# Kernel tuning notes

Hardware: AMD Instinct MI355X
Metric: run time of the kernel (lower is better)

## Reference

```python
import jax, jax.numpy as jnp
import numpy as np

NUM_HEADS = 8
MAX_POINTS = 8


def _sample_one(img, x, y):
    # img: [hd, Hs, Ws]; x, y: [N, P] pixel coords. Bilinear, zeros padding,
    # align_corners=True (caller already converted normalized coords to pixels).
    Hs, Ws = img.shape[-2], img.shape[-1]
    x0f = jnp.floor(x); y0f = jnp.floor(y)
    x0 = x0f.astype(jnp.int32); y0 = y0f.astype(jnp.int32)
    x1 = x0 + 1; y1 = y0 + 1
    wx1 = x - x0f; wx0 = 1.0 - wx1
    wy1 = y - y0f; wy0 = 1.0 - wy1

    def gather(yi, xi):
        valid = ((yi >= 0) & (yi < Hs) & (xi >= 0) & (xi < Ws)).astype(img.dtype)
        yc = jnp.clip(yi, 0, Hs - 1)
        xc = jnp.clip(xi, 0, Ws - 1)
        return img[:, yc, xc] * valid  # [hd, N, P]

    return (gather(y0, x0) * (wy0 * wx0) + gather(y0, x1) * (wy0 * wx1)
            + gather(y1, x0) * (wy1 * wx0) + gather(y1, x1) * (wy1 * wx1))


def _forward(query, ref, q_w, q_b, kv_w, kv_b, off_w, off_b, out_w, out_b, H, W, n_points):
    B, N, C = query.shape
    hd = C // NUM_HEADS
    scale = hd ** -0.5

    q = (query @ q_w + q_b).reshape(B, N, NUM_HEADS, hd)
    # kv_proj is dead code in the source forward (k, v are never used); params kept for parity.

    offsets = (query @ off_w + off_b).reshape(B, N, NUM_HEADS, MAX_POINTS, 2)
    offsets = offsets[:, :, :, :n_points]  # [B, N, nh, P, 2]

    ys = jnp.arange(H, dtype=query.dtype)
    xs = jnp.arange(W, dtype=query.dtype)
    coords = jnp.stack(jnp.meshgrid(ys, xs, indexing='ij'), -1).reshape(N, 2)  # (y, x)
    loc = coords[None, :, None, None, :] + offsets  # [B, N, nh, P, 2]
    g0 = loc[..., 0] / (H - 1) * 2.0 - 1.0
    g1 = loc[..., 1] / (W - 1) * 2.0 - 1.0
    # grid_sample reads grid[...,0] as x and grid[...,1] as y -> faithful to the
    # source's coordinate-channel ordering (channel 0 was normalized with H).
    x_pix = (g0 + 1.0) * 0.5 * (W - 1)
    y_pix = (g1 + 1.0) * 0.5 * (H - 1)

    ref_img = ref.reshape(B, C, H, W)  # faithful to source's .view (raw reinterpret, no permute)
    ref_heads = ref_img.reshape(B, NUM_HEADS, hd, H, W)  # per-head channel slice

    xb = x_pix.transpose(0, 2, 1, 3)  # [B, nh, N, P]
    yb = y_pix.transpose(0, 2, 1, 3)
    sampled = jax.vmap(jax.vmap(_sample_one))(ref_heads, xb, yb)  # [B, nh, hd, N, P]
    sampled = sampled.transpose(0, 3, 1, 4, 2)  # [B, N, nh, P, hd]

    attn = jax.nn.softmax(jnp.einsum('bnhd,bnhpd->bnhp', q, sampled) * scale, axis=-1)
    out = jnp.einsum('bnhp,bnhpd->bnhd', attn, sampled).reshape(B, N, C)
    return out @ out_w + out_b


def setup_inputs():
    key = jax.random.key(0)
    B, H, W, C = 4, 64, 64, 512
    N = H * W
    ks = jax.random.split(key, 8)
    w = lambda k, shp: jax.random.normal(k, shp, jnp.float32) * 0.02
    return {
        'query': jax.random.normal(ks[0], (B, N, C), jnp.float32),
        'ref': jax.random.normal(ks[1], (B, N, C), jnp.float32),
        'q_w': w(ks[2], (C, C)), 'q_b': jnp.zeros((C,), jnp.float32),
        'kv_w': w(ks[3], (C, 2 * C)), 'kv_b': jnp.zeros((2 * C,), jnp.float32),
        'off_w': w(ks[4], (C, NUM_HEADS * MAX_POINTS * 2)),
        'off_b': jnp.zeros((NUM_HEADS * MAX_POINTS * 2,), jnp.float32),
        'out_w': w(ks[5], (C, C)), 'out_b': jnp.zeros((C,), jnp.float32),
        'H': H, 'W': W, 'n_points': 8,
    }


def reference(query, ref, q_w, q_b, kv_w, kv_b, off_w, off_b, out_w, out_b, H, W, n_points):
    return _forward(query, ref, q_w, q_b, kv_w, kv_b, off_w, off_b, out_w, out_b, H, W, n_points)
```

## Files before the change

### kernel.cpp

```cpp
#include <hip/hip_runtime.h>
#include <cmath>

#define NUM_HEADS 8
#define MAX_POINTS 8
#define HD 64

typedef short bf16x8 __attribute__((ext_vector_type(8)));
typedef float f32x4 __attribute__((ext_vector_type(4)));
typedef float f32x2 __attribute__((ext_vector_type(2)));

typedef const __attribute__((address_space(1))) unsigned int gu32;
typedef __attribute__((address_space(3))) unsigned int lu32;

__device__ __forceinline__ unsigned short f2bf(float f) {
    unsigned u = __float_as_uint(f);
    unsigned r = (u + 0x7fff + ((u >> 16) & 1)) >> 16;
    return (unsigned short)r;
}
__device__ __forceinline__ unsigned packbf2(float a, float b) {
    return (unsigned)f2bf(a) | ((unsigned)f2bf(b) << 16);
}
__device__ __forceinline__ f32x2 bfpair(unsigned u) {
    f32x2 r;
    r.x = __uint_as_float(u << 16);
    r.y = __uint_as_float(u & 0xffff0000u);
    return r;
}
__device__ __forceinline__ f32x2 sp2(float v) { return (f32x2){v, v}; }
__device__ __forceinline__ f32x2 pkfma(f32x2 a, f32x2 b, f32x2 c) {
    f32x2 d;
    asm("v_pk_fma_f32 %0, %1, %2, %3" : "=v"(d) : "v"(a), "v"(b), "v"(c));
    return d;
}
__device__ __forceinline__ f32x2 pkmul(f32x2 a, f32x2 b) {
    f32x2 d;
    asm("v_pk_mul_f32 %0, %1, %2" : "=v"(d) : "v"(a), "v"(b));
    return d;
}

__global__ __launch_bounds__(256) void prep_k(
    const float* __restrict__ query, unsigned short* __restrict__ qin_bf,
    const float* __restrict__ ref, unsigned short* __restrict__ refT,
    const float* __restrict__ q_w, const float* __restrict__ off_w,
    const float* __restrict__ out_w, unsigned short* __restrict__ wcat,
    unsigned short* __restrict__ woutT)
{
    __shared__ float tile[32][33];
    int bid = blockIdx.x;
    int tid = threadIdx.x;

    if (bid < 8192) {
        int i = (bid * 256 + tid) * 4;
        float4 v = *(const float4*)&query[i];
        ushort4 o;
        o.x = f2bf(v.x); o.y = f2bf(v.y); o.z = f2bf(v.z); o.w = f2bf(v.w);
        *(ushort4*)&qin_bf[i] = o;
        return;
    }
    int tx = tid & 31, ty = tid >> 5;
    if (bid < 16384) {
        int b2 = bid - 8192;
        int z = b2 >> 11;
        int r = b2 & 2047;
        int k0 = (r & 15) * 32;
        int n0 = (r >> 4) * 32;
        size_t ib = (size_t)z * 512 * 4096;
#pragma unroll
        for (int i = 0; i < 32; i += 8)
            tile[ty + i][tx] = ref[ib + (size_t)(k0 + ty + i) * 4096 + n0 + tx];
        __syncthreads();
#pragma unroll
        for (int i = 0; i < 32; i += 8)
            refT[ib + (size_t)(n0 + ty + i) * 512 + k0 + tx] = f2bf(tile[tx][ty + i]);
        return;
    }
    int b3 = bid - 16384;
    int z = b3 >> 8;
    int r = b3 & 255;
    int k0 = (r & 15) * 32;
    int n0 = (r >> 4) * 32;
    const float* in; unsigned short* out; int N;
    if (z == 0)      { in = q_w;   out = wcat;             N = 512; }
    else if (z == 1) { in = off_w; out = wcat + 512 * 512; N = 128;
                       if (n0 >= 128) return; }
    else             { in = out_w; out = woutT;            N = 512; }
#pragma unroll
    for (int i = 0; i < 32; i += 8)
        tile[ty + i][tx] = in[(size_t)(k0 + ty + i) * N + n0 + tx];
    __syncthreads();
#pragma unroll
    for (int i = 0; i < 32; i += 8)
        out[(size_t)(n0 + ty + i) * 512 + k0 + tx] = f2bf(tile[tx][ty + i]);
}

__device__ __forceinline__ void gemm128_core(
    const unsigned short* A, const unsigned short* BT, int K,
    int bm, int bn, int tid, unsigned short* As, unsigned short* Bs,
    f32x4 (&acc)[4][4])
{
    int wave = tid >> 6, lane = tid & 63;
    int quad = lane >> 4, l16 = lane & 15;
    int wm = (wave >> 1) * 64, wn = (wave & 1) * 64;
    int srow = tid >> 2, sq = (tid & 3) * 8;
    const unsigned short* aP0 = &A[(size_t)(bm + srow) * K + sq];
    const unsigned short* aP1 = aP0 + (size_t)64 * K;
    const unsigned short* bP0 = &BT[(size_t)(bn + srow) * K + sq];
    const unsigned short* bP1 = bP0 + (size_t)64 * K;

#define STAGE(buf, k0)                                                         \
    do {                                                                       \
        lu32* aL0 = (lu32*)&As[(buf) * 4096 + wave * 512];                     \
        lu32* aL1 = (lu32*)&As[(buf) * 4096 + 2048 + wave * 512];              \
        lu32* bL0 = (lu32*)&Bs[(buf) * 4096 + wave * 512];                     \
        lu32* bL1 = (lu32*)&Bs[(buf) * 4096 + 2048 + wave * 512];              \
        __builtin_amdgcn_global_load_lds((gu32*)(aP0 + (k0)), aL0, 16, 0, 0);  \
        __builtin_amdgcn_global_load_lds((gu32*)(aP1 + (k0)), aL1, 16, 0, 0);  \
        __builtin_amdgcn_global_load_lds((gu32*)(bP0 + (k0)), bL0, 16, 0, 0);  \
        __builtin_amdgcn_global_load_lds((gu32*)(bP1 + (k0)), bL1, 16, 0, 0);  \
    } while (0)

    STAGE(0, 0);
    __syncthreads();
    int cur = 0;
    for (int k0 = 0; k0 < K; k0 += 32) {
        if (k0 + 32 < K) STAGE(cur ^ 1, k0 + 32);
        bf16x8 af[4], bfr[4];
#pragma unroll
        for (int t = 0; t < 4; ++t) {
            af[t]  = *(const bf16x8*)&As[cur * 4096 + (wm + t * 16 + l16) * 32 + quad * 8];
            bfr[t] = *(const bf16x8*)&Bs[cur * 4096 + (wn + t * 16 + l16) * 32 + quad * 8];
        }
#pragma unroll
        for (int mt = 0; mt < 4; ++mt)
#pragma unroll
            for (int nt = 0; nt < 4; ++nt)
                acc[mt][nt] = __builtin_amdgcn_mfma_f32_16x16x32_bf16(
                    af[mt], bfr[nt], acc[mt][nt], 0, 0, 0);
        __syncthreads();
        cur ^= 1;
    }
#undef STAGE
}

__global__ __launch_bounds__(256) void gemm_qoff_k(
    const unsigned short* __restrict__ A, const unsigned short* __restrict__ BT,
    const float* __restrict__ q_b, const float* __restrict__ off_b,
    unsigned short* __restrict__ qout, float* __restrict__ offout,
    int M, int K)
{
    __shared__ unsigned short As[2 * 128 * 32];
    __shared__ unsigned short Bs[2 * 128 * 32];
    int tid = threadIdx.x;
    int wave = tid >> 6, lane = tid & 63;
    int quad = lane >> 4, l16 = lane & 15;
    int bm = blockIdx.y * 128, bn = blockIdx.x * 128;
    int wm = (wave >> 1) * 64, wn = (wave & 1) * 64;

    f32x4 acc[4][4];
#pragma unroll
    for (int i = 0; i < 4; ++i)
#pragma unroll
        for (int j = 0; j < 4; ++j) acc[i][j] = (f32x4){0.f, 0.f, 0.f, 0.f};

    gemm128_core(A, BT, K, bm, bn, tid, As, Bs, acc);

#pragma unroll
    for (int mt = 0; mt < 4; ++mt)
#pragma unroll
        for (int nt = 0; nt < 4; ++nt) {
            int r0 = bm + wm + mt * 16 + quad * 4;
            int c  = bn + wn + nt * 16 + l16;
            if (bn < 512) {
                float bv = q_b[c];
#pragma unroll
                for (int r = 0; r < 4; ++r)
                    qout[(size_t)(r0 + r) * 512 + c] = f2bf(acc[mt][nt][r] + bv);
            } else {
                int co = c - 512;
                float bv = off_b[co];
#pragma unroll
                for (int r = 0; r < 4; ++r)
                    offout[(size_t)(r0 + r) * 128 + co] = acc[mt][nt][r] + bv;
            }
        }
}

__global__ __launch_bounds__(256) void gemm_out_k(
    const unsigned short* __restrict__ A, const unsigned short* __restrict__ BT,
    const float* __restrict__ bias, float* __restrict__ Cf, int M, int N, int K)
{
    __shared__ unsigned short As[2 * 128 * 32];
    __shared__ unsigned short Bs[2 * 128 * 32];
    int tid = threadIdx.x;
    int wave = tid >> 6, lane = tid & 63;
    int quad = lane >> 4, l16 = lane & 15;
    int bm = blockIdx.y * 128, bn = blockIdx.x * 128;
    int wm = (wave >> 1) * 64, wn = (wave & 1) * 64;

    f32x4 acc[4][4];
#pragma unroll
    for (int i = 0; i < 4; ++i)
#pragma unroll
        for (int j = 0; j < 4; ++j) acc[i][j] = (f32x4){0.f, 0.f, 0.f, 0.f};

    gemm128_core(A, BT, K, bm, bn, tid, As, Bs, acc);

#pragma unroll
    for (int mt = 0; mt < 4; ++mt)
#pragma unroll
        for (int nt = 0; nt < 4; ++nt) {
            int r0 = bm + wm + mt * 16 + quad * 4;
            int c  = bn + wn + nt * 16 + l16;
            float bv = bias[c];
#pragma unroll
            for (int r = 0; r < 4; ++r)
                Cf[(size_t)(r0 + r) * N + c] = acc[mt][nt][r] + bv;
        }
}

__global__ __launch_bounds__(256, 4) void sample_attn_sp_k(
    const unsigned short* __restrict__ qb, const float* __restrict__ offb,
    const unsigned short* __restrict__ refT, unsigned short* __restrict__ ob,
    const int* __restrict__ npp)
{
    __shared__ float slog[2][NUM_HEADS][MAX_POINTS];
    __shared__ f32x2 spart[2][4][64];
    int npts = *npp;
    int tid = threadIdx.x;
    int qsel = tid >> 7;
    int w = (tid >> 6) & 1;
    int lane = tid & 63;
    int h = lane >> 3;
    int j = lane & 7;
    int coff = (h << 6) + (j << 3);

    int bi = blockIdx.x;
    int grp = bi & 7;
    int b = grp >> 1;
    int idx = ((bi >> 3) << 1) | (grp & 1);
    int n = (idx << 1) | qsel;
    int bn = (b << 12) | n;
    int row = n >> 6, col = n & 63;

    uint4 qu = *(const uint4*)&qb[(bn << 9) + coff];
    f32x2 qv2[4] = {bfpair(qu.x), bfpair(qu.y), bfpair(qu.z), bfpair(qu.w)};

    const float* op = offb + (bn << 7) + (h << 4) + (w << 3);
    float4 of0 = *(const float4*)op;
    float4 of1 = *(const float4*)(op + 4);
    float ox[4] = {of0.x, of0.z, of1.x, of1.z};
    float oy[4] = {of0.y, of0.w, of1.y, of1.w};

    const unsigned short* rb = refT + ((size_t)b << 21) + coff;

    int ofs[4][4];
#pragma unroll
    for (int p = 0; p < 4; ++p) {
        float x = (float)row + ox[p];
        float y = (float)col + oy[p];
        int x0 = (int)floorf(x), y0 = (int)floorf(y);
        int yc0 = min(max(y0, 0), 63), yc1 = min(max(y0 + 1, 0), 63);
        int xc0 = min(max(x0, 0), 63), xc1 = min(max(x0 + 1, 0), 63);
        ofs[p][0] = ((yc0 << 6) + xc0) << 9;
        ofs[p][1] = ((yc0 << 6) + xc1) << 9;
        ofs[p][2] = ((yc1 << 6) + xc0) << 9;
        ofs[p][3] = ((yc1 << 6) + xc1) << 9;
    }
    uint4 u[4][4];
#pragma unroll
    for (int p = 0; p < 4; ++p)
#pragma unroll
        for (int c = 0; c < 4; ++c)
            u[p][c] = *(const uint4*)(rb + ofs[p][c]);

    f32x2 sv[4][4];
    float lg[4];
#pragma unroll
    for (int p = 0; p < 4; ++p) {
        float x = (float)row + ox[p];
        float y = (float)col + oy[p];
        float x0f = floorf(x), y0f = floorf(y);
        int x0 = (int)x0f, y0 = (int)y0f;
        float wx1 = x - x0f, wx0 = 1.f - wx1;
        float wy1 = y - y0f, wy0 = 1.f - wy1;
        float wya = ((unsigned)y0       < 64u) ? wy0 : 0.f;
        float wyb = ((unsigned)(y0 + 1) < 64u) ? wy1 : 0.f;
        float wxa = ((unsigned)x0       < 64u) ? wx0 : 0.f;
        float wxb = ((unsigned)(x0 + 1) < 64u) ? wx1 : 0.f;
        f32x2 w00 = sp2(wya * wxa), w01 = sp2(wya * wxb);
        f32x2 w10 = sp2(wyb * wxa), w11 = sp2(wyb * wxb);

        f32x2 a0 = pkmul(w00, bfpair(u[p][0].x));
        f32x2 a1 = pkmul(w00, bfpair(u[p][0].y));
        f32x2 a2 = pkmul(w00, bfpair(u[p][0].z));
        f32x2 a3 = pkmul(w00, bfpair(u[p][0].w));
        a0 = pkfma(w01, bfpair(u[p][1].x), a0);
        a1 = pkfma(w01, bfpair(u[p][1].y), a1);
        a2 = pkfma(w01, bfpair(u[p][1].z), a2);
        a3 = pkfma(w01, bfpair(u[p][1].w), a3);
        a0 = pkfma(w10, bfpair(u[p][2].x), a0);
        a1 = pkfma(w10, bfpair(u[p][2].y), a1);
        a2 = pkfma(w10, bfpair(u[p][2].z), a2);
        a3 = pkfma(w10, bfpair(u[p][2].w), a3);
        a0 = pkfma(w11, bfpair(u[p][3].x), a0);
        a1 = pkfma(w11, bfpair(u[p][3].y), a1);
        a2 = pkfma(w11, bfpair(u[p][3].z), a2);
        a3 = pkfma(w11, bfpair(u[p][3].w), a3);
        sv[p][0] = a0; sv[p][1] = a1; sv[p][2] = a2; sv[p][3] = a3;

        f32x2 t2 = pkmul(qv2[0], a0);
        t2 = pkfma(qv2[1], a1, t2);
        t2 = pkfma(qv2[2], a2, t2);
        t2 = pkfma(qv2[3], a3, t2);
        float t = t2.x + t2.y;
        t += __shfl_xor(t, 1);
        t += __shfl_xor(t, 2);
        t += __shfl_xor(t, 4);
        lg[p] = ((w * 4 + p) < npts) ? t * 0.125f : -1e30f;
    }

    int j3 = j & 3;
    float lgsel = (j3 == 0) ? lg[0] : (j3 == 1) ? lg[1] : (j3 == 2) ? lg[2] : lg[3];
    slog[qsel][h][w * 4 + j3] = lgsel;
    __syncthreads();

    float l8[8];
#pragma unroll
    for (int k = 0; k < 8; ++k) l8[k] = slog[qsel][h][k];
    float mx = -1e30f;
#pragma unroll
    for (int k = 0; k < 8; ++k) mx = fmaxf(mx, l8[k]);
    float ssum = 0.f;
#pragma unroll
    for (int k = 0; k < 8; ++k) {
        l8[k] = __expf(l8[k] - mx);
        ssum += l8[k];
    }
    float inv = 1.f / ssum;

    float lw[4];
#pragma unroll
    for (int i = 0; i < 4; ++i) lw[i] = w ? l8[4 + i] : l8[i];
    f32x2 lw0 = sp2(lw[0]), lw1 = sp2(lw[1]), lw2 = sp2(lw[2]), lw3 = sp2(lw[3]);

    f32x2 o2[4];
#pragma unroll
    for (int i = 0; i < 4; ++i) {
        f32x2 t = pkmul(lw0, sv[0][i]);
        t = pkfma(lw1, sv[1][i], t);
        t = pkfma(lw2, sv[2][i], t);
        t = pkfma(lw3, sv[3][i], t);
        o2[i] = t;
    }

    if (w == 1) {
#pragma unroll
        for (int i = 0; i < 4; ++i) spart[qsel][i][lane] = o2[i];
    }
    __syncthreads();
    if (w == 0) {
        f32x2 iv = sp2(inv);
#pragma unroll
        for (int i = 0; i < 4; ++i)
            o2[i] = pkmul(o2[i] + spart[qsel][i][lane], iv);
        uint4 o;
        o.x = packbf2(o2[0].x, o2[0].y);
        o.y = packbf2(o2[1].x, o2[1].y);
        o.z = packbf2(o2[2].x, o2[2].y);
        o.w = packbf2(o2[3].x, o2[3].y);
        *(uint4*)&ob[(bn << 9) + coff] = o;
    }
}

extern "C" void kernel_launch(void* const* d_in, const int* in_sizes, int n_in,
                              void* d_out, int out_size, void* d_ws, size_t ws_size,
                              hipStream_t stream) {
    const float* query = (const float*)d_in[0];
    const float* ref   = (const float*)d_in[1];
    const float* q_w   = (const float*)d_in[2];
    const float* q_b   = (const float*)d_in[3];
    const float* off_w = (const float*)d_in[6];
    const float* off_b = (const float*)d_in[7];
    const float* out_w = (const float*)d_in[8];
    const float* out_b = (const float*)d_in[9];
    const int* npp  = (const int*)d_in[12];

    const int C = 512;
    const int B = 4;
    const int N = 64 * 64;
    const int M = B * N;
    const int OFFD = NUM_HEADS * MAX_POINTS * 2;

    float* offbuf = (float*)d_ws;
    unsigned short* refT_bf = (unsigned short*)(offbuf + (size_t)M * OFFD);
    unsigned short* qin_bf  = refT_bf + (size_t)M * C;
    unsigned short* qbuf_bf = qin_bf  + (size_t)M * C;
    unsigned short* obuf_bf = qbuf_bf + (size_t)M * C;
    unsigned short* wcat    = obuf_bf + (size_t)M * C;
    unsigned short* woutT   = wcat + (size_t)(C + OFFD) * C;

    dim3 blk(256);
    prep_k<<<dim3(8192 + 8192 + 768), blk, 0, stream>>>(
        query, qin_bf, ref, refT_bf, q_w, off_w, out_w, wcat, woutT);

    gemm_qoff_k<<<dim3(5, M / 128), blk, 0, stream>>>(
        qin_bf, wcat, q_b, off_b, qbuf_bf, offbuf, M, C);

    sample_attn_sp_k<<<dim3(M / 2), blk, 0, stream>>>(
        qbuf_bf, offbuf, refT_bf, obuf_bf, npp);

    gemm_out_k<<<dim3(C / 128, M / 128), blk, 0, stream>>>(
        obuf_bf, woutT, out_b, (float*)d_out, M, C, C);
}
```

Baseline: 225.4 us.

## Recompute bilinear samples in second pass instead of holding them in registers

```diff
diff --git a/kernel.cpp b/kernel.cpp
--- a/kernel.cpp
+++ b/kernel.cpp
@@ -27,16 +27,6 @@
     return r;
 }
 __device__ __forceinline__ f32x2 sp2(float v) { return (f32x2){v, v}; }
-__device__ __forceinline__ f32x2 pkfma(f32x2 a, f32x2 b, f32x2 c) {
-    f32x2 d;
-    asm("v_pk_fma_f32 %0, %1, %2, %3" : "=v"(d) : "v"(a), "v"(b), "v"(c));
-    return d;
-}
-__device__ __forceinline__ f32x2 pkmul(f32x2 a, f32x2 b) {
-    f32x2 d;
-    asm("v_pk_mul_f32 %0, %1, %2" : "=v"(d) : "v"(a), "v"(b));
-    return d;
-}
 
 __global__ __launch_bounds__(256) void prep_k(
     const float* __restrict__ query, unsigned short* __restrict__ qin_bf,
@@ -218,7 +208,7 @@
         }
 }
 
-__global__ __launch_bounds__(256, 4) void sample_attn_sp_k(
+__global__ __launch_bounds__(256) void sample_attn_sp_k(
     const unsigned short* __restrict__ qb, const float* __restrict__ offb,
     const unsigned short* __restrict__ refT, unsigned short* __restrict__ ob,
     const int* __restrict__ npp)
@@ -242,9 +232,6 @@
     int bn = (b << 12) | n;
     int row = n >> 6, col = n & 63;
 
-    uint4 qu = *(const uint4*)&qb[(bn << 9) + coff];
-    f32x2 qv2[4] = {bfpair(qu.x), bfpair(qu.y), bfpair(qu.z), bfpair(qu.w)};
-
     const float* op = offb + (bn << 7) + (h << 4) + (w << 3);
     float4 of0 = *(const float4*)op;
     float4 of1 = *(const float4*)(op + 4);
@@ -253,27 +240,10 @@
 
     const unsigned short* rb = refT + ((size_t)b << 21) + coff;
 
-    int ofs[4][4];
-#pragma unroll
-    for (int p = 0; p < 4; ++p) {
-        float x = (float)row + ox[p];
-        float y = (float)col + oy[p];
-        int x0 = (int)floorf(x), y0 = (int)floorf(y);
-        int yc0 = min(max(y0, 0), 63), yc1 = min(max(y0 + 1, 0), 63);
-        int xc0 = min(max(x0, 0), 63), xc1 = min(max(x0 + 1, 0), 63);
-        ofs[p][0] = ((yc0 << 6) + xc0) << 9;
-        ofs[p][1] = ((yc0 << 6) + xc1) << 9;
-        ofs[p][2] = ((yc1 << 6) + xc0) << 9;
-        ofs[p][3] = ((yc1 << 6) + xc1) << 9;
-    }
-    uint4 u[4][4];
-#pragma unroll
-    for (int p = 0; p < 4; ++p)
-#pragma unroll
-        for (int c = 0; c < 4; ++c)
-            u[p][c] = *(const uint4*)(rb + ofs[p][c]);
-
-    f32x2 sv[4][4];
+    uint4 qu = *(const uint4*)&qb[(bn << 9) + coff];
+    f32x2 qv0 = bfpair(qu.x), qv1 = bfpair(qu.y);
+    f32x2 qv2 = bfpair(qu.z), qv3 = bfpair(qu.w);
+
     float lg[4];
 #pragma unroll
     for (int p = 0; p < 4; ++p) {
@@ -287,31 +257,39 @@
         float wyb = ((unsigned)(y0 + 1) < 64u) ? wy1 : 0.f;
         float wxa = ((unsigned)x0       < 64u) ? wx0 : 0.f;
         float wxb = ((unsigned)(x0 + 1) < 64u) ? wx1 : 0.f;
+        int yc0 = min(max(y0, 0), 63), yc1 = min(max(y0 + 1, 0), 63);
+        int xc0 = min(max(x0, 0), 63), xc1 = min(max(x0 + 1, 0), 63);
+        const unsigned short* ry0 = rb + (yc0 << 15);
+        const unsigned short* ry1 = rb + (yc1 << 15);
+        uint4 u00 = *(const uint4*)(ry0 + (xc0 << 9));
+        uint4 u01 = *(const uint4*)(ry0 + (xc1 << 9));
+        uint4 u10 = *(const uint4*)(ry1 + (xc0 << 9));
+        uint4 u11 = *(const uint4*)(ry1 + (xc1 << 9));
+
         f32x2 w00 = sp2(wya * wxa), w01 = sp2(wya * wxb);
         f32x2 w10 = sp2(wyb * wxa), w11 = sp2(wyb * wxb);
 
-        f32x2 a0 = pkmul(w00, bfpair(u[p][0].x));
-        f32x2 a1 = pkmul(w00, bfpair(u[p][0].y));
-        f32x2 a2 = pkmul(w00, bfpair(u[p][0].z));
-        f32x2 a3 = pkmul(w00, bfpair(u[p][0].w));
-        a0 = pkfma(w01, bfpair(u[p][1].x), a0);
-        a1 = pkfma(w01, bfpair(u[p][1].y), a1);
-        a2 = pkfma(w01, bfpair(u[p][1].z), a2);
-        a3 = pkfma(w01, bfpair(u[p][1].w), a3);
-        a0 = pkfma(w10, bfpair(u[p][2].x), a0);
-        a1 = pkfma(w10, bfpair(u[p][2].y), a1);
-        a2 = pkfma(w10, bfpair(u[p][2].z), a2);
-        a3 = pkfma(w10, bfpair(u[p][2].w), a3);
-        a0 = pkfma(w11, bfpair(u[p][3].x), a0);
-        a1 = pkfma(w11, bfpair(u[p][3].y), a1);
-        a2 = pkfma(w11, bfpair(u[p][3].z), a2);
-        a3 = pkfma(w11, bfpair(u[p][3].w), a3);
-        sv[p][0] = a0; sv[p][1] = a1; sv[p][2] = a2; sv[p][3] = a3;
-
-        f32x2 t2 = pkmul(qv2[0], a0);
-        t2 = pkfma(qv2[1], a1, t2);
-        t2 = pkfma(qv2[2], a2, t2);
-        t2 = pkfma(qv2[3], a3, t2);
+        f32x2 a0 = w00 * bfpair(u00.x);
+        f32x2 a1 = w00 * bfpair(u00.y);
+        f32x2 a2 = w00 * bfpair(u00.z);
+        f32x2 a3 = w00 * bfpair(u00.w);
+        a0 = __builtin_elementwise_fma(w01, bfpair(u01.x), a0);
+        a1 = __builtin_elementwise_fma(w01, bfpair(u01.y), a1);
+        a2 = __builtin_elementwise_fma(w01, bfpair(u01.z), a2);
+        a3 = __builtin_elementwise_fma(w01, bfpair(u01.w), a3);
+        a0 = __builtin_elementwise_fma(w10, bfpair(u10.x), a0);
+        a1 = __builtin_elementwise_fma(w10, bfpair(u10.y), a1);
+        a2 = __builtin_elementwise_fma(w10, bfpair(u10.z), a2);
+        a3 = __builtin_elementwise_fma(w10, bfpair(u10.w), a3);
+        a0 = __builtin_elementwise_fma(w11, bfpair(u11.x), a0);
+        a1 = __builtin_elementwise_fma(w11, bfpair(u11.y), a1);
+        a2 = __builtin_elementwise_fma(w11, bfpair(u11.z), a2);
+        a3 = __builtin_elementwise_fma(w11, bfpair(u11.w), a3);
+
+        f32x2 t2 = qv0 * a0;
+        t2 = __builtin_elementwise_fma(qv1, a1, t2);
+        t2 = __builtin_elementwise_fma(qv2, a2, t2);
+        t2 = __builtin_elementwise_fma(qv3, a3, t2);
         float t = t2.x + t2.y;
         t += __shfl_xor(t, 1);
         t += __shfl_xor(t, 2);
@@ -341,16 +319,51 @@
     float lw[4];
 #pragma unroll
     for (int i = 0; i < 4; ++i) lw[i] = w ? l8[4 + i] : l8[i];
-    f32x2 lw0 = sp2(lw[0]), lw1 = sp2(lw[1]), lw2 = sp2(lw[2]), lw3 = sp2(lw[3]);
 
     f32x2 o2[4];
 #pragma unroll
-    for (int i = 0; i < 4; ++i) {
-        f32x2 t = pkmul(lw0, sv[0][i]);
-        t = pkfma(lw1, sv[1][i], t);
-        t = pkfma(lw2, sv[2][i], t);
-        t = pkfma(lw3, sv[3][i], t);
-        o2[i] = t;
+    for (int i = 0; i < 4; ++i) o2[i] = (f32x2){0.f, 0.f};
+#pragma unroll
+    for (int p = 0; p < 4; ++p) {
+        float x = (float)row + ox[p];
+        float y = (float)col + oy[p];
+        float x0f = floorf(x), y0f = floorf(y);
+        int x0 = (int)x0f, y0 = (int)y0f;
+        float wx1 = x - x0f, wx0 = 1.f - wx1;
+        float wy1 = y - y0f, wy0 = 1.f - wy1;
+        float wya = ((unsigned)y0       < 64u) ? wy0 : 0.f;
+        float wyb = ((unsigned)(y0 + 1) < 64u) ? wy1 : 0.f;
+        float wxa = ((unsigned)x0       < 64u) ? wx0 : 0.f;
+        float wxb = ((unsigned)(x0 + 1) < 64u) ? wx1 : 0.f;
+        int yc0 = min(max(y0, 0), 63), yc1 = min(max(y0 + 1, 0), 63);
+        int xc0 = min(max(x0, 0), 63), xc1 = min(max(x0 + 1, 0), 63);
+        const unsigned short* ry0 = rb + (yc0 << 15);
+        const unsigned short* ry1 = rb + (yc1 << 15);
+        uint4 u00 = *(const uint4*)(ry0 + (xc0 << 9));
+        uint4 u01 = *(const uint4*)(ry0 + (xc1 << 9));
+        uint4 u10 = *(const uint4*)(ry1 + (xc0 << 9));
+        uint4 u11 = *(const uint4*)(ry1 + (xc1 << 9));
+
+        float lp = lw[p];
+        f32x2 w00 = sp2(wya * wxa * lp), w01 = sp2(wya * wxb * lp);
+        f32x2 w10 = sp2(wyb * wxa * lp), w11 = sp2(wyb * wxb * lp);
+
+        o2[0] = __builtin_elementwise_fma(w00, bfpair(u00.x), o2[0]);
+        o2[1] = __builtin_elementwise_fma(w00, bfpair(u00.y), o2[1]);
+        o2[2] = __builtin_elementwise_fma(w00, bfpair(u00.z), o2[2]);
+        o2[3] = __builtin_elementwise_fma(w00, bfpair(u00.w), o2[3]);
+        o2[0] = __builtin_elementwise_fma(w01, bfpair(u01.x), o2[0]);
+        o2[1] = __builtin_elementwise_fma(w01, bfpair(u01.y), o2[1]);
+        o2[2] = __builtin_elementwise_fma(w01, bfpair(u01.z), o2[2]);
+        o2[3] = __builtin_elementwise_fma(w01, bfpair(u01.w), o2[3]);
+        o2[0] = __builtin_elementwise_fma(w10, bfpair(u10.x), o2[0]);
+        o2[1] = __builtin_elementwise_fma(w10, bfpair(u10.y), o2[1]);
+        o2[2] = __builtin_elementwise_fma(w10, bfpair(u10.z), o2[2]);
+        o2[3] = __builtin_elementwise_fma(w10, bfpair(u10.w), o2[3]);
+        o2[0] = __builtin_elementwise_fma(w11, bfpair(u11.x), o2[0]);
+        o2[1] = __builtin_elementwise_fma(w11, bfpair(u11.y), o2[1]);
+        o2[2] = __builtin_elementwise_fma(w11, bfpair(u11.z), o2[2]);
+        o2[3] = __builtin_elementwise_fma(w11, bfpair(u11.w), o2[3]);
     }
 
     if (w == 1) {
@@ -362,7 +375,7 @@
         f32x2 iv = sp2(inv);
 #pragma unroll
         for (int i = 0; i < 4; ++i)
-            o2[i] = pkmul(o2[i] + spart[qsel][i][lane], iv);
+            o2[i] = (o2[i] + spart[qsel][i][lane]) * iv;
         uint4 o;
         o.x = packbf2(o2[0].x, o2[0].y);
         o.y = packbf2(o2[1].x, o2[1].y);
```

Result: no change. 223.6 us (-0.8%).
